# Kernel optimization log

Measured on AMD Instinct MI355X. Metric: run time of the kernel, lower is better.

## Reference

```python
import jax, jax.numpy as jnp
import numpy as np

NUM_LAYERS = 32
IN_SIZE = 1024
OUT_SIZE = 1024
B, S = 32, 256


def setup_inputs() -> dict:
    key = jax.random.key(0)
    k1, k2, k3 = jax.random.split(key, 3)
    x = jax.random.normal(k1, (B, S, IN_SIZE), dtype=jnp.float32)
    layer_idx = jax.random.randint(k2, (S,), 0, NUM_LAYERS, dtype=jnp.int32)
    # learned parameter: per-layer weight [L, O, D], normal(stddev=1.0) as in flax init
    weight = jax.random.normal(k3, (NUM_LAYERS, OUT_SIZE, IN_SIZE), dtype=jnp.float32)
    return {"x": x, "layer_idx": layer_idx, "weight": weight}


def reference(x, layer_idx, weight):
    # x: [B, S, D]; layer_idx: [S]; weight: [L, O, D]
    # Each sequence position s uses expert weight[layer_idx[s]]:
    #   out[b, s, o] = sum_d x[b, s, d] * weight[layer_idx[s], o, d]
    w = weight[layer_idx]                      # [S, O, D] gather
    return jnp.einsum('bsd,sod->bso', x, w)    # [B, S, O]
```

## Files before the change

kernel.cpp:

```cpp
#include <hip/hip_runtime.h>
#include <stdint.h>

#define NLAYERS 32
#define DSIZE   1024
#define OSIZE   1024
#define BATCH   32
#define SEQ     256

#define WS_PERM  16
#define WS_TILE  512
#define CHUNK    8
#define BK       32
#define TM       256
#define TN       128
#define THREADS  512
#define KITERS   (DSIZE / BK)

typedef __attribute__((ext_vector_type(8)))  short short8;
typedef __attribute__((ext_vector_type(16))) float f32x16;
typedef __attribute__((ext_vector_type(4)))  unsigned uint4v;

__global__ void prep_kernel(const int* __restrict__ layer_idx, int* __restrict__ wsi) {
    __shared__ int cnt[NLAYERS];
    __shared__ int start_[NLAYERS];
    __shared__ int cursor[NLAYERS];
    const int t = threadIdx.x;
    if (t < NLAYERS) cnt[t] = 0;
    __syncthreads();
    int l = 0;
    if (t < SEQ) { l = layer_idx[t]; atomicAdd(&cnt[l], 1); }
    __syncthreads();
    if (t == 0) {
        int acc = 0;
        for (int i = 0; i < NLAYERS; ++i) { start_[i] = acc; cursor[i] = acc; acc += cnt[i]; }
    }
    __syncthreads();
    if (t < SEQ) {
        int r = atomicAdd(&cursor[l], 1);
        wsi[WS_PERM + r] = t;
    }
    if (t == 0) {
        int nc = 0;
        for (int i = 0; i < NLAYERS; ++i) {
            const int c = cnt[i];
            for (int j = 0; j < c; j += CHUNK) {
                wsi[WS_TILE + nc*4 + 0] = i;
                wsi[WS_TILE + nc*4 + 1] = start_[i] + j;
                wsi[WS_TILE + nc*4 + 2] = (c - j < CHUNK) ? (c - j) : CHUNK;
                ++nc;
            }
        }
        wsi[0] = nc;
    }
}

static __device__ __forceinline__ unsigned pk2(float a, float b) {
    unsigned ua = __builtin_bit_cast(unsigned, a) + 0x8000u;
    unsigned ub = __builtin_bit_cast(unsigned, b) + 0x8000u;
    return __builtin_amdgcn_perm(ub, ua, 0x07060302u);
}

__global__ __launch_bounds__(THREADS, 4) void gemm_kernel(
        const float* __restrict__ x, const float* __restrict__ wgt,
        const int* __restrict__ wsi, float* __restrict__ out) {
    const int fid = blockIdx.x;
    const int xcd = fid & 7;
    const int u   = fid >> 3;
    const int g   = ((u >> 3) << 3) | xcd;
    const int ntile = u & 7;
    const int nchunks = wsi[0];
    if (g >= nchunks) return;
    const int layer     = wsi[WS_TILE + g*4 + 0];
    const int rank_base = wsi[WS_TILE + g*4 + 1];
    const int nranks    = wsi[WS_TILE + g*4 + 2];

    __shared__ __align__(16) short ldsA[2][TM * BK];
    __shared__ __align__(16) short ldsB[2][TN * BK];

    const int t    = threadIdx.x;
    const int slot = t & 3;
    const int rb   = t >> 2;
    const int wsw  = ((slot ^ (rb & 3)) << 3);

    const float* aptr[2];
    bool av[2];
    #pragma unroll
    for (int p = 0; p < 2; ++p) {
        const int r  = rb + 128*p;
        const int ro = r >> 5;
        const int b  = r & 31;
        av[p] = (ro < nranks);
        const int s = av[p] ? wsi[WS_PERM + rank_base + ro] : 0;
        aptr[p] = x + (((size_t)(b * SEQ + s)) << 10) + slot*8;
    }
    const float* bptr = wgt + ((size_t)layer << 20)
                            + (((size_t)(ntile * TN + rb)) << 10) + slot*8;

    float4 ra[2][2], rbv[2];
    auto load_step = [&](int kk) {
        #pragma unroll
        for (int p = 0; p < 2; ++p) {
            if (av[p]) {
                ra[p][0] = *(const float4*)(aptr[p] + kk);
                ra[p][1] = *(const float4*)(aptr[p] + kk + 4);
            }
        }
        rbv[0] = *(const float4*)(bptr + kk);
        rbv[1] = *(const float4*)(bptr + kk + 4);
    };
    auto store_to = [&](int buf) {
        #pragma unroll
        for (int p = 0; p < 2; ++p) {
            if (av[p]) {
                uint4v u4;
                u4.x = pk2(ra[p][0].x, ra[p][0].y);
                u4.y = pk2(ra[p][0].z, ra[p][0].w);
                u4.z = pk2(ra[p][1].x, ra[p][1].y);
                u4.w = pk2(ra[p][1].z, ra[p][1].w);
                *(uint4v*)&ldsA[buf][(rb + 128*p) * BK + wsw] = u4;
            }
        }
        {
            uint4v u4;
            u4.x = pk2(rbv[0].x, rbv[0].y);
            u4.y = pk2(rbv[0].z, rbv[0].w);
            u4.z = pk2(rbv[1].x, rbv[1].y);
            u4.w = pk2(rbv[1].z, rbv[1].w);
            *(uint4v*)&ldsB[buf][rb * BK + wsw] = u4;
        }
    };

    const int lane = t & 63;
    const int wv   = t >> 6;
    const int l31  = lane & 31;
    const int lh   = lane >> 5;
    const int wm   = (wv >> 1) << 6;
    const int wn   = (wv & 1) << 6;
    const int rsw  = l31 & 3;

    const int baseA0 = (wm +  0 + l31) * BK;
    const int baseA1 = (wm + 32 + l31) * BK;
    const int baseB0 = (wn +  0 + l31) * BK;
    const int baseB1 = (wn + 32 + l31) * BK;

    const int rank0 = wm >> 5;
    const bool ok0 = (rank0 + 0) < nranks;
    const bool ok1 = (rank0 + 1) < nranks;

    f32x16 acc[2][2];
    #pragma unroll
    for (int mi = 0; mi < 2; ++mi)
        #pragma unroll
        for (int ni = 0; ni < 2; ++ni)
            #pragma unroll
            for (int r = 0; r < 16; ++r) acc[mi][ni][r] = 0.f;

    load_step(0);
    store_to(0);
    __syncthreads();

    #pragma unroll 1
    for (int kt = 0; kt < KITERS; ++kt) {
        const int cur = kt & 1;
        const bool more = (kt + 1 < KITERS);
        if (more) load_step((kt + 1) * BK);
        #pragma unroll
        for (int sub = 0; sub < 2; ++sub) {
            const int gx = (((sub << 1) | lh) ^ rsw) << 3;
            short8 b0 = *(const short8*)&ldsB[cur][baseB0 + gx];
            short8 b1 = *(const short8*)&ldsB[cur][baseB1 + gx];
            if (ok0) {
                short8 a0 = *(const short8*)&ldsA[cur][baseA0 + gx];
                acc[0][0] = __builtin_amdgcn_mfma_f32_32x32x16_bf16(a0, b0, acc[0][0], 0, 0, 0);
                acc[0][1] = __builtin_amdgcn_mfma_f32_32x32x16_bf16(a0, b1, acc[0][1], 0, 0, 0);
            }
            if (ok1) {
                short8 a1 = *(const short8*)&ldsA[cur][baseA1 + gx];
                acc[1][0] = __builtin_amdgcn_mfma_f32_32x32x16_bf16(a1, b0, acc[1][0], 0, 0, 0);
                acc[1][1] = __builtin_amdgcn_mfma_f32_32x32x16_bf16(a1, b1, acc[1][1], 0, 0, 0);
            }
        }
        if (more) {
            store_to(cur ^ 1);
            __syncthreads();
        }
    }

    #pragma unroll
    for (int mi = 0; mi < 2; ++mi) {
        const int ro = rank0 + mi;
        if (ro < nranks) {
            const int s = wsi[WS_PERM + rank_base + ro];
            #pragma unroll
            for (int ni = 0; ni < 2; ++ni) {
                const int ocol = ntile * TN + wn + ni*32 + l31;
                #pragma unroll
                for (int r = 0; r < 16; ++r) {
                    const int brow = (r & 3) + 8*(r >> 2) + 4*lh;
                    out[(((size_t)(brow * SEQ + s)) << 10) + ocol] = acc[mi][ni][r];
                }
            }
        }
    }
}

extern "C" void kernel_launch(void* const* d_in, const int* in_sizes, int n_in,
                              void* d_out, int out_size, void* d_ws, size_t ws_size,
                              hipStream_t stream) {
    const float* x         = (const float*)d_in[0];
    const int*   layer_idx = (const int*)  d_in[1];
    const float* weight    = (const float*)d_in[2];
    float* out = (float*)d_out;
    int*   wsi = (int*)d_ws;

    prep_kernel<<<1, 256, 0, stream>>>(layer_idx, wsi);
    gemm_kernel<<<512, THREADS, 0, stream>>>(x, weight, wsi, out);
}
```

Before: 275.2 us.

## Halve per-chunk sequence tile to four positions and interleave LDS stores with MFMA

Chunks now hold four sequence positions instead of eight. The M tile drops from 256 to 128 rows, and each block uses 256 threads, with each thread loading two B rows. The grid is sized to the worst-case chunk count, and the XCD-aware block remap is replaced with a plain chunk/ntile split. The LDS swizzle is keyed on row pairs, and the A and B stores are split around the two MFMA sub-steps to overlap LDS writes with compute. The aim is less padding waste in partially filled chunks and more blocks for occupancy. The cost is that each layer's weight tile is re-read by more chunks, and the cross-XCD cache locality from the old remap is lost.

```diff
diff --git a/kernel.cpp b/kernel.cpp
--- a/kernel.cpp
+++ b/kernel.cpp
@@ -9,11 +9,12 @@
 
 #define WS_PERM  16
 #define WS_TILE  512
-#define CHUNK    8
+#define CHUNK    4
+#define MAXC     88
 #define BK       32
-#define TM       256
+#define TM       128
 #define TN       128
-#define THREADS  512
+#define THREADS  256
 #define KITERS   (DSIZE / BK)
 
 typedef __attribute__((ext_vector_type(8)))  short short8;
@@ -63,11 +64,9 @@
 __global__ __launch_bounds__(THREADS, 4) void gemm_kernel(
         const float* __restrict__ x, const float* __restrict__ wgt,
         const int* __restrict__ wsi, float* __restrict__ out) {
-    const int fid = blockIdx.x;
-    const int xcd = fid & 7;
-    const int u   = fid >> 3;
-    const int g   = ((u >> 3) << 3) | xcd;
-    const int ntile = u & 7;
+    const int fid   = blockIdx.x;
+    const int g     = fid >> 3;
+    const int ntile = fid & 7;
     const int nchunks = wsi[0];
     if (g >= nchunks) return;
     const int layer     = wsi[WS_TILE + g*4 + 0];
@@ -80,13 +79,13 @@
     const int t    = threadIdx.x;
     const int slot = t & 3;
     const int rb   = t >> 2;
-    const int wsw  = ((slot ^ (rb & 3)) << 3);
+    const int wsw  = ((slot ^ ((rb >> 1) & 3)) << 3);
 
     const float* aptr[2];
     bool av[2];
     #pragma unroll
     for (int p = 0; p < 2; ++p) {
-        const int r  = rb + 128*p;
+        const int r  = rb + 64*p;
         const int ro = r >> 5;
         const int b  = r & 31;
         av[p] = (ro < nranks);
@@ -96,7 +95,7 @@
     const float* bptr = wgt + ((size_t)layer << 20)
                             + (((size_t)(ntile * TN + rb)) << 10) + slot*8;
 
-    float4 ra[2][2], rbv[2];
+    float4 ra[2][2], rbv[2][2];
     auto load_step = [&](int kk) {
         #pragma unroll
         for (int p = 0; p < 2; ++p) {
@@ -105,10 +104,13 @@
                 ra[p][1] = *(const float4*)(aptr[p] + kk + 4);
             }
         }
-        rbv[0] = *(const float4*)(bptr + kk);
-        rbv[1] = *(const float4*)(bptr + kk + 4);
+        #pragma unroll
+        for (int p = 0; p < 2; ++p) {
+            rbv[p][0] = *(const float4*)(bptr + ((size_t)p << 16) + kk);
+            rbv[p][1] = *(const float4*)(bptr + ((size_t)p << 16) + kk + 4);
+        }
     };
-    auto store_to = [&](int buf) {
+    auto storeA = [&](int buf) {
         #pragma unroll
         for (int p = 0; p < 2; ++p) {
             if (av[p]) {
@@ -117,16 +119,19 @@
                 u4.y = pk2(ra[p][0].z, ra[p][0].w);
                 u4.z = pk2(ra[p][1].x, ra[p][1].y);
                 u4.w = pk2(ra[p][1].z, ra[p][1].w);
-                *(uint4v*)&ldsA[buf][(rb + 128*p) * BK + wsw] = u4;
-            }
-        }
-        {
+                *(uint4v*)&ldsA[buf][(rb + 64*p) * BK + wsw] = u4;
+            }
+        }
+    };
+    auto storeB = [&](int buf) {
+        #pragma unroll
+        for (int p = 0; p < 2; ++p) {
             uint4v u4;
-            u4.x = pk2(rbv[0].x, rbv[0].y);
-            u4.y = pk2(rbv[0].z, rbv[0].w);
-            u4.z = pk2(rbv[1].x, rbv[1].y);
-            u4.w = pk2(rbv[1].z, rbv[1].w);
-            *(uint4v*)&ldsB[buf][rb * BK + wsw] = u4;
+            u4.x = pk2(rbv[p][0].x, rbv[p][0].y);
+            u4.y = pk2(rbv[p][0].z, rbv[p][0].w);
+            u4.z = pk2(rbv[p][1].x, rbv[p][1].y);
+            u4.w = pk2(rbv[p][1].z, rbv[p][1].w);
+            *(uint4v*)&ldsB[buf][(rb + 64*p) * BK + wsw] = u4;
         }
     };
 
@@ -134,16 +139,16 @@
     const int wv   = t >> 6;
     const int l31  = lane & 31;
     const int lh   = lane >> 5;
-    const int wm   = (wv >> 1) << 6;
-    const int wn   = (wv & 1) << 6;
-    const int rsw  = l31 & 3;
-
-    const int baseA0 = (wm +  0 + l31) * BK;
-    const int baseA1 = (wm + 32 + l31) * BK;
-    const int baseB0 = (wn +  0 + l31) * BK;
-    const int baseB1 = (wn + 32 + l31) * BK;
-
-    const int rank0 = wm >> 5;
+    const int am   = (wv >> 1) << 6;
+    const int bn   = (wv & 1) << 6;
+    const int rsw  = (l31 >> 1) & 3;
+
+    const int baseA0 = (am +  0 + l31) * BK;
+    const int baseA1 = (am + 32 + l31) * BK;
+    const int baseB0 = (bn +  0 + l31) * BK;
+    const int baseB1 = (bn + 32 + l31) * BK;
+
+    const int rank0 = am >> 5;
     const bool ok0 = (rank0 + 0) < nranks;
     const bool ok1 = (rank0 + 1) < nranks;
 
@@ -156,7 +161,8 @@
             for (int r = 0; r < 16; ++r) acc[mi][ni][r] = 0.f;
 
     load_step(0);
-    store_to(0);
+    storeA(0);
+    storeB(0);
     __syncthreads();
 
     #pragma unroll 1
@@ -164,9 +170,8 @@
         const int cur = kt & 1;
         const bool more = (kt + 1 < KITERS);
         if (more) load_step((kt + 1) * BK);
-        #pragma unroll
-        for (int sub = 0; sub < 2; ++sub) {
-            const int gx = (((sub << 1) | lh) ^ rsw) << 3;
+        {
+            const int gx = ((0*2 + lh) ^ rsw) << 3;
             short8 b0 = *(const short8*)&ldsB[cur][baseB0 + gx];
             short8 b1 = *(const short8*)&ldsB[cur][baseB1 + gx];
             if (ok0) {
@@ -180,8 +185,24 @@
                 acc[1][1] = __builtin_amdgcn_mfma_f32_32x32x16_bf16(a1, b1, acc[1][1], 0, 0, 0);
             }
         }
+        if (more) storeA(cur ^ 1);
+        {
+            const int gx = ((1*2 + lh) ^ rsw) << 3;
+            short8 b0 = *(const short8*)&ldsB[cur][baseB0 + gx];
+            short8 b1 = *(const short8*)&ldsB[cur][baseB1 + gx];
+            if (ok0) {
+                short8 a0 = *(const short8*)&ldsA[cur][baseA0 + gx];
+                acc[0][0] = __builtin_amdgcn_mfma_f32_32x32x16_bf16(a0, b0, acc[0][0], 0, 0, 0);
+                acc[0][1] = __builtin_amdgcn_mfma_f32_32x32x16_bf16(a0, b1, acc[0][1], 0, 0, 0);
+            }
+            if (ok1) {
+                short8 a1 = *(const short8*)&ldsA[cur][baseA1 + gx];
+                acc[1][0] = __builtin_amdgcn_mfma_f32_32x32x16_bf16(a1, b0, acc[1][0], 0, 0, 0);
+                acc[1][1] = __builtin_amdgcn_mfma_f32_32x32x16_bf16(a1, b1, acc[1][1], 0, 0, 0);
+            }
+        }
         if (more) {
-            store_to(cur ^ 1);
+            storeB(cur ^ 1);
             __syncthreads();
         }
     }
@@ -193,7 +214,7 @@
             const int s = wsi[WS_PERM + rank_base + ro];
             #pragma unroll
             for (int ni = 0; ni < 2; ++ni) {
-                const int ocol = ntile * TN + wn + ni*32 + l31;
+                const int ocol = ntile * TN + bn + ni*32 + l31;
                 #pragma unroll
                 for (int r = 0; r < 16; ++r) {
                     const int brow = (r & 3) + 8*(r >> 2) + 4*lh;
@@ -214,5 +235,5 @@
     int*   wsi = (int*)d_ws;
 
     prep_kernel<<<1, 256, 0, stream>>>(layer_idx, wsi);
-    gemm_kernel<<<512, THREADS, 0, stream>>>(x, weight, wsi, out);
-}
+    gemm_kernel<<<MAXC * 8, THREADS, 0, stream>>>(x, weight, wsi, out);
+}
```

Measured after the change: 282.6 us. +2.7%, slower.
